# Kernel optimization log

Hardware: AMD Instinct MI355X
Metric: run time of the kernel (lower is better)

## Reference

```python
import jax, jax.numpy as jnp
import numpy as np

DIM = 512
N_LABELS = 64


def setup_inputs() -> dict:
    key = jax.random.key(0)
    k1, k2, k3, k4 = jax.random.split(key, 4)
    head = jax.random.normal(k1, (8, 512, DIM), dtype=jnp.float32)
    dep = jax.random.normal(k2, (8, 512, DIM), dtype=jnp.float32)
    label_W = jax.random.normal(k3, (N_LABELS, 2 * DIM), dtype=jnp.float32) * 0.02
    label_b = jax.random.normal(k4, (N_LABELS,), dtype=jnp.float32) * 0.02
    return {"head": head, "dep": dep, "label_W": label_W, "label_b": label_b}


def reference(head, dep, label_W, label_b):
    # Original: concated[b, i*S+j] = concat(head[b,i], dep[b,j]) -> [B, S*S, 2D]
    #           out = (label_W @ concated^T).view(B, L, S, S) + b
    # Fused biaffine decomposition: out[b,l,i,j] = Wh[l].head[b,i] + Wd[l].dep[b,j] + b[l]
    D = head.shape[-1]
    W_head = label_W[:, :D]   # [L, D]
    W_dep = label_W[:, D:]    # [L, D]
    h = jnp.einsum('bid,ld->bli', head, W_head)  # [B, L, S]
    d = jnp.einsum('bjd,ld->blj', dep, W_dep)    # [B, L, S]
    out = h[:, :, :, None] + d[:, :, None, :] + label_b[None, :, None, None]
    return out  # [B, L, S, S]
```

## Files before the change

### kernel.cpp

```cpp
#include <hip/hip_runtime.h>
#include <hip/hip_bf16.h>

#define BATCH 8
#define SEQ   512
#define DIM   512
#define NL    64

typedef float f32x4 __attribute__((ext_vector_type(4)));

__global__ __launch_bounds__(256) void alab_wt(
    const float* __restrict__ W, f32x4* __restrict__ wt4)
{
    const int tid = blockIdx.x * 256 + threadIdx.x;
    const int l   = tid & 63;
    const int k4  = (tid >> 6) & 127;
    const int hd  = tid >> 13;
    wt4[tid] = *(const f32x4*)(W + (size_t)l * (2 * DIM) + hd * DIM + k4 * 4);
}

__global__ __launch_bounds__(256) void alab_proj4(
    const float* __restrict__ head, const float* __restrict__ dep,
    const f32x4* __restrict__ wt4, const float* __restrict__ bias,
    float* __restrict__ hbuf, float* __restrict__ dbuf)
{
    __shared__ f32x4 srow[16][128];
    const int bid   = blockIdx.x;
    const int hd    = bid & 1;
    const int itile = (bid >> 1) & 31;
    const int b     = bid >> 6;
    const int i0    = itile * 16;

    const float* src = hd ? dep  : head;
    float*       dst = hd ? dbuf : hbuf;

    const f32x4* s4 = (const f32x4*)(src + ((size_t)b * SEQ + i0) * DIM);
    #pragma unroll
    for (int u = threadIdx.x; u < 16 * 128; u += 256)
        srow[u >> 7][u & 127] = s4[u];
    __syncthreads();

    const int lane = threadIdx.x & 63;
    const int w    = threadIdx.x >> 6;

    const f32x4* wbase = wt4 + (size_t)hd * 128 * 64 + lane;
    f32x4 a0 = {0,0,0,0}, a1 = {0,0,0,0}, a2 = {0,0,0,0}, a3 = {0,0,0,0};
    #pragma unroll 4
    for (int k4 = 0; k4 < 128; ++k4) {
        const f32x4 wt = wbase[(size_t)k4 * 64];
        a0 += srow[w * 4 + 0][k4] * wt;
        a1 += srow[w * 4 + 1][k4] * wt;
        a2 += srow[w * 4 + 2][k4] * wt;
        a3 += srow[w * 4 + 3][k4] * wt;
    }
    const float bb = hd ? 0.f : bias[lane];
    f32x4 r = { a0.x + a0.y + a0.z + a0.w + bb,
                a1.x + a1.y + a1.z + a1.w + bb,
                a2.x + a2.y + a2.z + a2.w + bb,
                a3.x + a3.y + a3.z + a3.w + bb };
    *(f32x4*)(dst + ((size_t)b * NL + lane) * SEQ + i0 + w * 4) = r;
}

__global__ __launch_bounds__(256) void alab_bcast4(
    const float* __restrict__ hbuf, const float* __restrict__ dbuf,
    float* __restrict__ out)
{
    __shared__ float sh[SEQ];
    __shared__ f32x4 sd4[SEQ / 4];
    const int t  = threadIdx.x;
    const int bl = blockIdx.x;

    sh[t]                  = hbuf[(size_t)bl * SEQ + t];
    sh[t + 256]            = hbuf[(size_t)bl * SEQ + t + 256];
    ((float*)sd4)[t]       = dbuf[(size_t)bl * SEQ + t];
    ((float*)sd4)[t + 256] = dbuf[(size_t)bl * SEQ + t + 256];
    __syncthreads();

    const int j4 = t & 127;
    const int rh = t >> 7;
    const f32x4 dreg = sd4[j4];
    f32x4* ob = (f32x4*)out + (size_t)bl * SEQ * (SEQ / 4);

    #pragma unroll 8
    for (int ii = 0; ii < SEQ; ii += 2) {
        const int i = ii + rh;
        ob[(size_t)i * (SEQ / 4) + j4] = dreg + sh[i];
    }
}

extern "C" void kernel_launch(void* const* d_in, const int* in_sizes, int n_in,
                              void* d_out, int out_size, void* d_ws, size_t ws_size,
                              hipStream_t stream) {
    const float* head = (const float*)d_in[0];
    const float* dep  = (const float*)d_in[1];
    const float* W    = (const float*)d_in[2];
    const float* bias = (const float*)d_in[3];
    float* out = (float*)d_out;

    const size_t P = (size_t)BATCH * NL * SEQ;
    float* hbuf = (float*)d_ws;
    float* dbuf = hbuf + P;
    f32x4* wt4  = (f32x4*)(dbuf + P);

    alab_wt   <<<64,         256, 0, stream>>>(W, wt4);
    alab_proj4<<<BATCH * 64, 256, 0, stream>>>(head, dep, wt4, bias, hbuf, dbuf);
    alab_bcast4<<<BATCH * NL, 256, 0, stream>>>(hbuf, dbuf, out);
}
```

Baseline: 119.6 us.

## Compute head/dep projections with bf16 MFMA instead of fp32 FMA loops

Converts the weights and input rows to bf16 (round-to-nearest-even) and computes the projection GEMM with 16x16x32 bf16 MFMA instructions. The weight pre-transform now writes bf16 in row-major [hd][l][k] layout, and the LDS tile is padded to reduce bank conflicts. This targets the projection stage's scalar FMA cost, but lowers input precision to bf16. The output write stage, which dominates memory traffic at 64MB, is unchanged.

```diff
diff --git a/kernel.cpp b/kernel.cpp
--- a/kernel.cpp
+++ b/kernel.cpp
@@ -7,23 +7,34 @@
 #define NL    64
 
 typedef float f32x4 __attribute__((ext_vector_type(4)));
+using bf16x8 = __attribute__((ext_vector_type(8))) short;
 
-__global__ __launch_bounds__(256) void alab_wt(
-    const float* __restrict__ W, f32x4* __restrict__ wt4)
+static __device__ __forceinline__ unsigned bf1(float f) {
+    unsigned u = __builtin_bit_cast(unsigned, f);
+    return (u + 0x7FFFu + ((u >> 16) & 1u)) >> 16;
+}
+static __device__ __forceinline__ unsigned bfpair(float a, float b) {
+    return bf1(a) | (bf1(b) << 16);
+}
+
+__global__ __launch_bounds__(256) void alab_wt2(
+    const float* __restrict__ W, unsigned short* __restrict__ wbf)
 {
     const int tid = blockIdx.x * 256 + threadIdx.x;
-    const int l   = tid & 63;
-    const int k4  = (tid >> 6) & 127;
     const int hd  = tid >> 13;
-    wt4[tid] = *(const f32x4*)(W + (size_t)l * (2 * DIM) + hd * DIM + k4 * 4);
+    const int l   = (tid >> 7) & 63;
+    const int kc  = (tid & 127) * 4;
+    const float4 f = *(const float4*)(W + (size_t)l * (2 * DIM) + hd * DIM + kc);
+    uint2 o = { bfpair(f.x, f.y), bfpair(f.z, f.w) };
+    *(uint2*)(wbf + ((size_t)hd * NL + l) * DIM + kc) = o;
 }
 
-__global__ __launch_bounds__(256) void alab_proj4(
+__global__ __launch_bounds__(256) void alab_proj6(
     const float* __restrict__ head, const float* __restrict__ dep,
-    const f32x4* __restrict__ wt4, const float* __restrict__ bias,
+    const unsigned short* __restrict__ wbf, const float* __restrict__ bias,
     float* __restrict__ hbuf, float* __restrict__ dbuf)
 {
-    __shared__ f32x4 srow[16][128];
+    __shared__ __align__(16) unsigned short A_lds[16 * 520];
     const int bid   = blockIdx.x;
     const int hd    = bid & 1;
     const int itile = (bid >> 1) & 31;
@@ -33,31 +44,44 @@
     const float* src = hd ? dep  : head;
     float*       dst = hd ? dbuf : hbuf;
 
-    const f32x4* s4 = (const f32x4*)(src + ((size_t)b * SEQ + i0) * DIM);
+    const float* arow = src + ((size_t)b * SEQ + i0) * DIM;
     #pragma unroll
-    for (int u = threadIdx.x; u < 16 * 128; u += 256)
-        srow[u >> 7][u & 127] = s4[u];
+    for (int u = threadIdx.x; u < 1024; u += 256) {
+        const int row = u >> 6, kc = (u & 63) * 8;
+        const float* p = arow + row * DIM + kc;
+        const float4 f0 = *(const float4*)p;
+        const float4 f1 = *(const float4*)(p + 4);
+        uint4 wv = { bfpair(f0.x, f0.y), bfpair(f0.z, f0.w),
+                     bfpair(f1.x, f1.y), bfpair(f1.z, f1.w) };
+        *(uint4*)&A_lds[row * 520 + kc] = wv;
+    }
     __syncthreads();
 
     const int lane = threadIdx.x & 63;
     const int w    = threadIdx.x >> 6;
+    const int lr   = lane & 15;
+    const int kg   = lane >> 4;
 
-    const f32x4* wbase = wt4 + (size_t)hd * 128 * 64 + lane;
-    f32x4 a0 = {0,0,0,0}, a1 = {0,0,0,0}, a2 = {0,0,0,0}, a3 = {0,0,0,0};
-    #pragma unroll 4
-    for (int k4 = 0; k4 < 128; ++k4) {
-        const f32x4 wt = wbase[(size_t)k4 * 64];
-        a0 += srow[w * 4 + 0][k4] * wt;
-        a1 += srow[w * 4 + 1][k4] * wt;
-        a2 += srow[w * 4 + 2][k4] * wt;
-        a3 += srow[w * 4 + 3][k4] * wt;
+    const unsigned short* Ab = &A_lds[lr * 520 + kg * 8];
+    const unsigned short* Bb = wbf + ((size_t)hd * NL + w * 16 + lr) * DIM + kg * 8;
+
+    f32x4 acc0 = {0.f, 0.f, 0.f, 0.f}, acc1 = {0.f, 0.f, 0.f, 0.f};
+    #pragma unroll
+    for (int s = 0; s < 16; s += 2) {
+        const bf16x8 a0 = *(const bf16x8*)(Ab + (s + 0) * 32);
+        const bf16x8 b0 = *(const bf16x8*)(Bb + (s + 0) * 32);
+        const bf16x8 a1 = *(const bf16x8*)(Ab + (s + 1) * 32);
+        const bf16x8 b1 = *(const bf16x8*)(Bb + (s + 1) * 32);
+        acc0 = __builtin_amdgcn_mfma_f32_16x16x32_bf16(a0, b0, acc0, 0, 0, 0);
+        acc1 = __builtin_amdgcn_mfma_f32_16x16x32_bf16(a1, b1, acc1, 0, 0, 0);
     }
-    const float bb = hd ? 0.f : bias[lane];
-    f32x4 r = { a0.x + a0.y + a0.z + a0.w + bb,
-                a1.x + a1.y + a1.z + a1.w + bb,
-                a2.x + a2.y + a2.z + a2.w + bb,
-                a3.x + a3.y + a3.z + a3.w + bb };
-    *(f32x4*)(dst + ((size_t)b * NL + lane) * SEQ + i0 + w * 4) = r;
+    const f32x4 acc = acc0 + acc1;
+
+    const int l = w * 16 + lr;
+    const int i = i0 + kg * 4;
+    const float bb = hd ? 0.f : bias[l];
+    const f32x4 r = acc + bb;
+    *(f32x4*)(dst + ((size_t)b * NL + l) * SEQ + i) = r;
 }
 
 __global__ __launch_bounds__(256) void alab_bcast4(
@@ -99,9 +123,9 @@
     const size_t P = (size_t)BATCH * NL * SEQ;
     float* hbuf = (float*)d_ws;
     float* dbuf = hbuf + P;
-    f32x4* wt4  = (f32x4*)(dbuf + P);
+    unsigned short* wbf = (unsigned short*)(dbuf + P);
 
-    alab_wt   <<<64,         256, 0, stream>>>(W, wt4);
-    alab_proj4<<<BATCH * 64, 256, 0, stream>>>(head, dep, wt4, bias, hbuf, dbuf);
+    alab_wt2  <<<64,         256, 0, stream>>>(W, wbf);
+    alab_proj6<<<BATCH * 64, 256, 0, stream>>>(head, dep, wbf, bias, hbuf, dbuf);
     alab_bcast4<<<BATCH * NL, 256, 0, stream>>>(hbuf, dbuf, out);
 }
```

Measured after the change: 110.7 us. -7.5%, faster.
